# Performance work log

Measured on AMD Instinct MI355X. Metric: run time of the kernel, lower is better.

The kernel has to match this reference:

```python
import jax, jax.numpy as jnp
import numpy as np
from jax import lax

SCORE_THRESH = 0.05
NMS_THRESH = 0.5
DET_PER_IMG = 100
K_PRE = 2048  # pre-NMS candidate cap (batched_nms is never run on N*C dense candidates)
BBOX_XFORM_CLIP = float(np.log(1000.0 / 16.0))
WX, WY, WW, WH = 10.0, 10.0, 5.0, 5.0


def _decode(reg, props):
    # reg: [N, C, 4] deltas, props: [N, 4] xyxy -> [N, C, 4] xyxy (torchvision BoxCoder.decode)
    w = props[:, 2] - props[:, 0]
    h = props[:, 3] - props[:, 1]
    cx = props[:, 0] + 0.5 * w
    cy = props[:, 1] + 0.5 * h
    dx = reg[..., 0] / WX
    dy = reg[..., 1] / WY
    dw = jnp.minimum(reg[..., 2] / WW, BBOX_XFORM_CLIP)
    dh = jnp.minimum(reg[..., 3] / WH, BBOX_XFORM_CLIP)
    pcx = dx * w[:, None] + cx[:, None]
    pcy = dy * h[:, None] + cy[:, None]
    pw = jnp.exp(dw) * w[:, None]
    ph = jnp.exp(dh) * h[:, None]
    return jnp.stack([pcx - 0.5 * pw, pcy - 0.5 * ph, pcx + 0.5 * pw, pcy + 0.5 * ph], axis=-1)


def _pairwise_iou(b):
    # b: [K, 4] -> [K, K]
    area = (b[:, 2] - b[:, 0]) * (b[:, 3] - b[:, 1])
    lt = jnp.maximum(b[:, None, :2], b[None, :, :2])
    rb = jnp.minimum(b[:, None, 2:], b[None, :, 2:])
    wh = jnp.clip(rb - lt, 0.0)
    inter = wh[..., 0] * wh[..., 1]
    return inter / (area[:, None] + area[None, :] - inter)


def _greedy_nms(iou, valid, thresh):
    # boxes assumed sorted by descending score; valid: [K] bool initial keep mask
    K = iou.shape[0]
    idx = jnp.arange(K)
    def body(i, keep):
        sup = (iou[i] > thresh) & (idx > i) & keep[i]
        return keep & (~sup)
    return lax.fori_loop(0, K, body, valid)


def _process_image(logits, reg, props, img_h, img_w):
    # logits: [N, C], reg: [N, 4C], props: [N, 4]
    N, C = logits.shape
    scores = jax.nn.softmax(logits, axis=-1)[:, 1:]          # [N, C-1] drop background
    boxes = _decode(reg.reshape(N, C, 4), props)[:, 1:]      # [N, C-1, 4]
    boxes = jnp.stack([
        jnp.clip(boxes[..., 0], 0.0, img_w),
        jnp.clip(boxes[..., 1], 0.0, img_h),
        jnp.clip(boxes[..., 2], 0.0, img_w),
        jnp.clip(boxes[..., 3], 0.0, img_h),
    ], axis=-1)
    labels = jnp.broadcast_to(jnp.arange(1, C), (N, C - 1))
    boxes = boxes.reshape(-1, 4)       # [M, 4], M = N*(C-1)
    scores = scores.reshape(-1)
    labels = labels.reshape(-1)
    wd = boxes[:, 2] - boxes[:, 0]
    ht = boxes[:, 3] - boxes[:, 1]
    valid = (scores > SCORE_THRESH) & (wd >= 1.0) & (ht >= 1.0)  # score thresh + remove_small_boxes
    masked = jnp.where(valid, scores, -1.0)
    top_s, top_i = lax.top_k(masked, K_PRE)
    tb = boxes[top_i]
    tl = labels[top_i]
    tvalid = top_s > SCORE_THRESH
    # batched_nms via per-class coordinate offsets
    off = tl.astype(tb.dtype) * (jnp.max(tb) + 1.0)
    keep = _greedy_nms(_pairwise_iou(tb + off[:, None]), tvalid, NMS_THRESH)
    ks = jnp.where(keep, top_s, -1.0)
    fs, fi = lax.top_k(ks, DET_PER_IMG)
    fvalid = fs > SCORE_THRESH
    out_boxes = jnp.where(fvalid[:, None], tb[fi], 0.0)
    out_scores = jnp.where(fvalid, fs, 0.0)
    out_labels = jnp.where(fvalid, tl[fi], -1)
    return out_boxes, out_scores, out_labels


def setup_inputs() -> dict:
    key = jax.random.key(0)
    k1, k2, k3 = jax.random.split(key, 3)
    B, N, C, H, W = 8, 4000, 91, 800, 800
    pts = jax.random.uniform(k1, (B, N, 2, 2), dtype=jnp.float32, minval=0.0, maxval=float(W))
    proposals = jnp.concatenate([pts.min(axis=2), pts.max(axis=2)], axis=-1)  # valid xyxy
    class_logits = jax.random.normal(k2, (B * N, C), dtype=jnp.float32)
    box_regression = 0.5 * jax.random.normal(k3, (B * N, 4 * C), dtype=jnp.float32)
    return {"class_logits": class_logits, "box_regression": box_regression,
            "proposals": proposals, "img_h": H, "img_w": W}


def reference(class_logits, box_regression, proposals, img_h, img_w):
    B, N, _ = proposals.shape
    C = class_logits.shape[-1]
    logits = class_logits.reshape(B, N, C)
    reg = box_regression.reshape(B, N, 4 * C)
    fn = lambda l, r, p: _process_image(l, r, p, float(img_h), float(img_w))
    boxes, scores, labels = jax.vmap(fn)(logits, reg, proposals)
    return boxes, scores, labels
```

## Files before the change

### kernel.cpp

```cpp
#include <hip/hip_runtime.h>
#include <stdint.h>

typedef unsigned int u32;
typedef unsigned long long u64;
typedef __attribute__((ext_vector_type(2))) unsigned long long u64x2;

#define BIMG 8
#define NPROP 4000
#define NCLS 91
#define CM1 90
#define MCAND (NPROP * CM1)
#define KPRE 2048
#define NBUCKET 4096
#define NREP 8
#define SELCAP 16384
#define NSLOT 32
#define DETS 100
#define WLCAP 2048
#define SCORE_T 0.05f
#define NMS_T 0.5f
#define BBOX_CLIP 4.135166556742356f

#define HISTREP_OFF ((size_t)0)
#define BCNTREP_OFF (HISTREP_OFF + (size_t)NREP * BIMG * NBUCKET * 4)
#define META_OFF    (BCNTREP_OFF + (size_t)NREP * BIMG * NBUCKET * 4)
#define ZERO_BYTES  (META_OFF + 4096)
#define START_OFF   (ZERO_BYTES)
#define HISTTOT_OFF (START_OFF + (size_t)BIMG * NBUCKET * 4)
#define STARTREP_OFF (HISTTOT_OFF + (size_t)BIMG * NBUCKET * 4)
#define SEL_OFF     (STARTREP_OFF + (size_t)NREP * BIMG * NBUCKET * 4)
#define TBOX_OFF    (SEL_OFF + (size_t)BIMG * SELCAP * 8)
#define TSB_OFF     (TBOX_OFF + (size_t)BIMG * KPRE * 16)
#define TSC_OFF     (TSB_OFF + (size_t)BIMG * KPRE * 16)
#define TLB_OFF     (TSC_OFF + (size_t)BIMG * KPRE * 4)
#define TVLB_OFF    (TLB_OFF + (size_t)BIMG * KPRE * 4)
#define WLIST_OFF   (TVLB_OFF + (size_t)BIMG * 32 * 8)
#define CLIST_OFF   (WLIST_OFF + (size_t)BIMG * WLCAP * 4)
#define CVALID_OFF  (CLIST_OFF + (size_t)BIMG * NPROP * NSLOT * 8)
#define MASK_OFF    (CVALID_OFF + (size_t)BIMG * NPROP * 2 * 8)
#define WS_NEED     (MASK_OFF + (size_t)BIMG * KPRE * 32 * 8)

__device__ __forceinline__ void decode_clip(const float4 rg, const float w, const float h,
                                            const float cx, const float cy,
                                            const float fw, const float fh, float bx[4]) {
    float dx = rg.x / 10.0f;
    float dy = rg.y / 10.0f;
    float dw = fminf(rg.z / 5.0f, BBOX_CLIP);
    float dh = fminf(rg.w / 5.0f, BBOX_CLIP);
    float pcx = dx * w + cx;
    float pcy = dy * h + cy;
    float pw  = expf(dw) * w;
    float phh = expf(dh) * h;
    bx[0] = fminf(fmaxf(pcx - 0.5f * pw,  0.0f), fw);
    bx[1] = fminf(fmaxf(pcy - 0.5f * phh, 0.0f), fh);
    bx[2] = fminf(fmaxf(pcx + 0.5f * pw,  0.0f), fw);
    bx[3] = fminf(fmaxf(pcy + 0.5f * phh, 0.0f), fh);
}

__global__ __launch_bounds__(256) void k1_score_hist(
    const float* __restrict__ logits, const float* __restrict__ reg,
    const float* __restrict__ props, const int* __restrict__ imh, const int* __restrict__ imw,
    u32* __restrict__ histrep, u64* __restrict__ clist, u64* __restrict__ cvalid) {
    const int lane = threadIdx.x & 63;
    const int pid = blockIdx.x * 4 + (threadIdx.x >> 6);
    if (pid >= BIMG * NPROP) return;
    const int img = pid / NPROP;
    const float fw = (float)imw[0], fh = (float)imh[0];
    const float* lrow = logits + (size_t)pid * NCLS;
    float v0 = lrow[lane];
    float v1 = (lane < 27) ? lrow[lane + 64] : -3.0e38f;
    float mx = fmaxf(v0, v1);
#pragma unroll
    for (int o = 32; o > 0; o >>= 1) mx = fmaxf(mx, __shfl_xor(mx, o));
    float es = expf(v0 - mx) + ((lane < 27) ? expf(v1 - mx) : 0.0f);
#pragma unroll
    for (int o = 32; o > 0; o >>= 1) es += __shfl_xor(es, o);
    const float thr = mx + logf(es) - 2.9967323f;
    float4 p = reinterpret_cast<const float4*>(props)[pid];
    const float w = p.z - p.x, h = p.w - p.y;
    const float cx = p.x + 0.5f * w, cy = p.y + 0.5f * h;
    const float4* rrow = reinterpret_cast<const float4*>(reg) + (size_t)pid * NCLS;
    const int n = pid - img * NPROP;
    const int rep = n & (NREP - 1);
    const float sh0 = __shfl(v0, (lane + 1) & 63);
    const float sh1 = __shfl(v1, (lane + 1) & 63);
    u64 w0 = 0ull, w1 = 0ull;
    u32 base1 = 0;
#pragma unroll
    for (int batch = 0; batch < 2; ++batch) {
        const int ci = lane + batch * 64;
        bool valid = false;
        u32 ob = 0u;
        if (ci < CM1) {
            const float l = (batch == 0) ? ((lane == 63) ? sh1 : sh0) : sh1;
            if (l > thr) {
                float sc = expf(l - mx) / es;
                float4 rg = rrow[ci + 1];
                float bx[4];
                decode_clip(rg, w, h, cx, cy, fw, fh, bx);
                valid = (sc > SCORE_T) && (bx[2] - bx[0] >= 1.0f) && (bx[3] - bx[1] >= 1.0f);
                if (valid) {
                    ob = __float_as_uint(sc) | 0x80000000u;
                    atomicAdd(&histrep[((size_t)img * NREP + rep) * NBUCKET + (ob >> 20)], 1u);
                }
            }
        }
        const u64 bal = __ballot(valid);
        if (batch == 0) { w0 = bal; base1 = (u32)__popcll(bal); }
        else            { w1 = bal; }
        if (valid) {
            const u32 pre = (u32)__popcll(bal & ((1ull << lane) - 1ull));
            const u32 slot = (batch == 0) ? pre : (base1 + pre);
            const u32 idx = (u32)n * CM1 + (u32)ci;
            clist[(size_t)pid * NSLOT + slot] = ((u64)ob << 32) | (u32)(~idx);
        }
    }
    if (lane == 0) {
        u64x2 v; v.x = w0; v.y = w1;
        reinterpret_cast<u64x2*>(cvalid)[pid] = v;
    }
}

__global__ __launch_bounds__(256) void k2_scan(
    const u32* __restrict__ histrep, u32* __restrict__ histtot,
    u32* __restrict__ start, u32* __restrict__ startrep, u32* __restrict__ meta,
    u32* __restrict__ wlist) {
    __shared__ u32 wsum[4], qws[4];
    __shared__ u32 TbkS, Vs;
    const int img = blockIdx.x;
    const int td = threadIdx.x;
    const int ln = td & 63, wv = td >> 6;
    const int lo = 4080 - td * 16;
    u32 cnt[16];
#pragma unroll
    for (int k = 0; k < 16; ++k) cnt[k] = 0;
    const u32* hb = histrep + (size_t)img * NREP * NBUCKET + lo;
#pragma unroll
    for (int r = 0; r < NREP; ++r) {
        const uint4* q = reinterpret_cast<const uint4*>(hb + (size_t)r * NBUCKET);
        uint4 a = q[0], b = q[1], c = q[2], d = q[3];
        cnt[15] += a.x; cnt[14] += a.y; cnt[13] += a.z; cnt[12] += a.w;
        cnt[11] += b.x; cnt[10] += b.y; cnt[9]  += b.z; cnt[8]  += b.w;
        cnt[7]  += c.x; cnt[6]  += c.y; cnt[5]  += c.z; cnt[4]  += c.w;
        cnt[3]  += d.x; cnt[2]  += d.y; cnt[1]  += d.z; cnt[0]  += d.w;
    }
    u32 tsum = 0;
#pragma unroll
    for (int k = 0; k < 16; ++k) tsum += cnt[k];
    u32 inc = tsum;
#pragma unroll
    for (int o = 1; o < 64; o <<= 1) { u32 t = __shfl_up(inc, o); if (ln >= o) inc += t; }
    if (td == 0) TbkS = 0u;
    if (ln == 63) wsum[wv] = inc;
    __syncthreads();
    u32 wbase = 0;
    for (int i = 0; i < wv; ++i) wbase += wsum[i];
    if (td == 255) Vs = wbase + inc;
    const u32 excl0 = wbase + inc - tsum;
    u32 sub[16];
    u32 excl = excl0;
#pragma unroll
    for (int k = 0; k < 16; ++k) {
        const int bk = 4095 - (td * 16 + k);
        start[img * NBUCKET + bk] = excl;
        histtot[img * NBUCKET + bk] = cnt[k];
        sub[k] = excl;
        if (cnt[k] > 0 && excl < KPRE && excl + cnt[k] >= KPRE) TbkS = (u32)bk;
        excl += cnt[k];
    }
#pragma unroll
    for (int r = 0; r < NREP; ++r) {
        const uint4* q = reinterpret_cast<const uint4*>(hb + (size_t)r * NBUCKET);
        uint4 a = q[0], b = q[1], c = q[2], d = q[3];
        u32 hh[16] = { d.w, d.z, d.y, d.x, c.w, c.z, c.y, c.x,
                       b.w, b.z, b.y, b.x, a.w, a.z, a.y, a.x };
#pragma unroll
        for (int k = 0; k < 16; ++k) {
            const int bk = 4095 - (td * 16 + k);
            startrep[((size_t)img * NBUCKET + bk) * NREP + r] = sub[k];
            sub[k] += hh[k];
        }
    }
    u32 qcnt = 0;
    {
        u32 e = excl0;
#pragma unroll
        for (int k = 0; k < 16; ++k) { if (cnt[k] >= 2 && e < KPRE) ++qcnt; e += cnt[k]; }
    }
    u32 qinc = qcnt;
#pragma unroll
    for (int o = 1; o < 64; o <<= 1) { u32 t = __shfl_up(qinc, o); if (ln >= o) qinc += t; }
    if (ln == 63) qws[wv] = qinc;
    __syncthreads();
    u32 qbase = 0;
    for (int i = 0; i < wv; ++i) qbase += qws[i];
    u32 qoff = qbase + qinc - qcnt;
    {
        u32 e = excl0;
#pragma unroll
        for (int k = 0; k < 16; ++k) {
            const int bk = 4095 - (td * 16 + k);
            if (cnt[k] >= 2 && e < KPRE && qoff < WLCAP) wlist[img * WLCAP + (qoff++)] = (u32)bk;
            e += cnt[k];
        }
    }
    if (td == 255) meta[img * 8 + 3] = qbase + qinc;
    __syncthreads();
    if (td == 0) {
        u32 V = Vs;
        meta[img * 8 + 0] = V;
        meta[img * 8 + 1] = TbkS;
        meta[img * 8 + 2] = (V < KPRE) ? (KPRE - V) : 0u;
    }
}

__global__ __launch_bounds__(256) void k3_compact(
    const u64* __restrict__ clist, const u64* __restrict__ cvalid,
    const u32* __restrict__ startrep, const u32* __restrict__ meta,
    u32* __restrict__ bcntrep, u64* __restrict__ sel) {
    const u32 t = blockIdx.x * 256 + threadIdx.x;
    const u32 row = t >> 2;
    const u32 s0 = t & 3;
    if (row < (u32)(BIMG * NPROP)) {
        const u64x2 vb = reinterpret_cast<const u64x2*>(cvalid)[row];
        const u32 rcnt = (u32)__popcll(vb.x) + (u32)__popcll(vb.y);
        if (s0 < rcnt) {
            const u32 img = row / NPROP;
            const u32 n = row - img * NPROP;
            const u32 rep = n & (NREP - 1);
            const u32 cutoff = meta[img * 8 + 1];
            for (u32 slot = s0; slot < rcnt; slot += 4) {
                const u64 e = clist[(size_t)row * NSLOT + slot];
                const u32 bk = (u32)(e >> 52);
                if (bk >= cutoff) {
                    const u32 pos = startrep[((size_t)img * NBUCKET + bk) * NREP + rep] +
                        atomicAdd(&bcntrep[((size_t)rep * BIMG + img) * NBUCKET + bk], 1u);
                    if (pos < SELCAP) sel[(size_t)img * SELCAP + pos] = e;
                }
            }
        }
    }
    if (blockIdx.x < BIMG && threadIdx.x < 64) {
        const int img = blockIdx.x;
        const u32 need = meta[img * 8 + 2];
        if (need != 0) {
            const u32 V = meta[img * 8 + 0];
            const int lv = threadIdx.x;
            const u32 ORDN1 = 0x407FFFFFu;
            u32 filled = 0;
            for (u32 b0 = 0; b0 < MCAND && filled < need; b0 += 64) {
                const u32 idx = b0 + (u32)lv;
                bool inv = false;
                if (idx < MCAND) {
                    const u32 nn = (u32)(((u64)idx * 3054198967ull) >> 38);
                    const u32 cq = idx - nn * 90u;
                    const u64 wb = cvalid[((size_t)img * NPROP + nn) * 2 + (cq >> 6)];
                    inv = ((wb >> (cq & 63)) & 1ull) == 0ull;
                }
                const u64 bal = __ballot(inv);
                const u32 pre = (u32)__popcll(bal & ((1ull << lv) - 1ull));
                if (inv && (filled + pre) < need)
                    sel[(size_t)img * SELCAP + V + filled + pre] =
                        ((u64)ORDN1 << 32) | (u32)(~idx);
                filled += (u32)__popcll(bal);
            }
        }
    }
}

__global__ __launch_bounds__(256) void k4_sortseg(
    const u32* __restrict__ histtot, const u32* __restrict__ start,
    const u32* __restrict__ meta, const u32* __restrict__ wlist, u64* __restrict__ sel) {
    __shared__ u64 arr[4096];
    const int img = blockIdx.y;
    const int tid = threadIdx.x;
    const u32 wcount = meta[img * 8 + 3];
    for (u32 wi = blockIdx.x; wi < wcount; wi += gridDim.x) {
        const u32 bk = (wi < WLCAP) ? wlist[img * WLCAP + wi] : 0u;
        u32 cnt = histtot[img * NBUCKET + bk];
        u32 st = start[img * NBUCKET + bk];
        if (cnt <= 64 || st >= KPRE) continue;
        if (st + cnt > SELCAP) cnt = SELCAP - st;
        if (cnt > 4096) cnt = 4096;
        int n = 1;
        while (n < (int)cnt) n <<= 1;
        u64* seg = sel + (size_t)img * SELCAP + st;
        for (int i = tid; i < n; i += 256) arr[i] = (i < (int)cnt) ? seg[i] : 0ull;
        __syncthreads();
        for (int k = 2; k <= n; k <<= 1)
            for (int j = k >> 1; j > 0; j >>= 1) {
                for (int i = tid; i < n; i += 256) {
                    int ixj = i ^ j;
                    if (ixj > i) {
                        u64 a = arr[i], b = arr[ixj];
                        bool swp = ((i & k) == 0) ? (a < b) : (a > b);
                        if (swp) { arr[i] = b; arr[ixj] = a; }
                    }
                }
                __syncthreads();
            }
        for (int i = tid; i < (int)cnt; i += 256) seg[i] = arr[i];
        __syncthreads();
    }
    const int wv = tid >> 6, lane = tid & 63;
    for (u32 wi = blockIdx.x * 4 + wv; wi < wcount; wi += gridDim.x * 4) {
        const u32 bk = (wi < WLCAP) ? wlist[img * WLCAP + wi] : 0u;
        u32 cnt = histtot[img * NBUCKET + bk];
        u32 st = start[img * NBUCKET + bk];
        if (cnt < 2 || cnt > 64 || st >= KPRE) continue;
        if (st + cnt > SELCAP) cnt = SELCAP - st;
        u64* seg = sel + (size_t)img * SELCAP + st;
        u64 key = (lane < (int)cnt) ? seg[lane] : 0ull;
#pragma unroll
        for (int k = 2; k <= 64; k <<= 1) {
#pragma unroll
            for (int j = k >> 1; j > 0; j >>= 1) {
                u64 other = __shfl_xor(key, j);
                bool takeMax = ((lane & j) == 0) == ((lane & k) == 0);
                u64 hi2 = (key > other) ? key : other;
                u64 lo2 = (key > other) ? other : key;
                key = takeMax ? hi2 : lo2;
            }
        }
        if (lane < (int)cnt) seg[lane] = key;
    }
}

__global__ __launch_bounds__(1024) void k5_gather(
    const u64* __restrict__ sel, const float* __restrict__ reg, const float* __restrict__ props,
    const int* __restrict__ imh, const int* __restrict__ imw,
    float* __restrict__ tbox, float* __restrict__ tsb, float* __restrict__ tsc,
    int* __restrict__ tlb, u64* __restrict__ tvlb) {
    const int img = blockIdx.x;
    const int tid = threadIdx.x;
    const float fw = (float)imw[0], fh = (float)imh[0];
    float bx[2][4];
    int lab[2];
    float lm = -3.0e38f;
#pragma unroll
    for (int t = 0; t < 2; ++t) {
        int s = t * 1024 + tid;
        u64 key = sel[(size_t)img * SELCAP + s];
        u32 o = (u32)(key >> 32);
        u32 idx = ~((u32)key);
        u32 b = (o & 0x80000000u) ? (o & 0x7FFFFFFFu) : ~o;
        float sc = __uint_as_float(b);
        u32 n = idx / CM1;
        int c = (int)(idx - n * CM1) + 1;
        int pid = img * NPROP + (int)n;
        float4 p = reinterpret_cast<const float4*>(props)[pid];
        float w = p.z - p.x, h = p.w - p.y;
        float cx = p.x + 0.5f * w, cy = p.y + 0.5f * h;
        float4 rg = reinterpret_cast<const float4*>(reg)[(size_t)pid * NCLS + c];
        decode_clip(rg, w, h, cx, cy, fw, fh, bx[t]);
        lab[t] = c;
        lm = fmaxf(lm, fmaxf(fmaxf(bx[t][0], bx[t][1]), fmaxf(bx[t][2], bx[t][3])));
        reinterpret_cast<float4*>(tbox)[(size_t)img * KPRE + s] =
            make_float4(bx[t][0], bx[t][1], bx[t][2], bx[t][3]);
        tsc[(size_t)img * KPRE + s] = sc;
        tlb[(size_t)img * KPRE + s] = c;
        u64 bw = __ballot(sc > SCORE_T);
        if ((tid & 63) == 0) tvlb[img * 32 + t * 16 + (tid >> 6)] = bw;
    }
#pragma unroll
    for (int o2 = 32; o2 > 0; o2 >>= 1) lm = fmaxf(lm, __shfl_xor(lm, o2));
    __shared__ float wm[16];
    if ((tid & 63) == 0) wm[tid >> 6] = lm;
    __syncthreads();
    float m = wm[0];
#pragma unroll
    for (int i = 1; i < 16; ++i) m = fmaxf(m, wm[i]);
    const float mplus = m + 1.0f;
#pragma unroll
    for (int t = 0; t < 2; ++t) {
        int s = t * 1024 + tid;
        float off = (float)lab[t] * mplus;
        reinterpret_cast<float4*>(tsb)[(size_t)img * KPRE + s] =
            make_float4(bx[t][0] + off, bx[t][1] + off, bx[t][2] + off, bx[t][3] + off);
    }
}

__global__ __launch_bounds__(256) void k6_mask(
    const float* __restrict__ tsb, u64* __restrict__ mask) {
    const int img = blockIdx.y;
    const int wv = threadIdx.x >> 6, lane = threadIdx.x & 63;
    const u32 t = blockIdx.x * 4 + wv;
    float f = sqrtf(8.0f * (float)t + 1.0f);
    u32 x = (u32)((f - 1.0f) * 0.5f);
    while ((x + 1) * (x + 2) / 2 <= t) ++x;
    while (x * (x + 1) / 2 > t) --x;
    const u32 y = t - x * (x + 1) / 2;
    const int j0 = (int)x * 64;
    const int i0 = (int)y * 64;
    __shared__ float4 cb[4][64];
    __shared__ float ca[4][64];
    float4 c = reinterpret_cast<const float4*>(tsb)[(size_t)img * KPRE + j0 + lane];
    cb[wv][lane] = c;
    ca[wv][lane] = (c.z - c.x) * (c.w - c.y);
    __syncthreads();
    const int i = i0 + lane;
    float4 r = reinterpret_cast<const float4*>(tsb)[(size_t)img * KPRE + i];
    float ra = (r.z - r.x) * (r.w - r.y);
    u64 bits = 0ull;
#pragma unroll 8
    for (int jj = 0; jj < 64; ++jj) {
        int j = j0 + jj;
        float4 cc = cb[wv][jj];
        float wvv = fmaxf(fminf(r.z, cc.z) - fmaxf(r.x, cc.x), 0.0f);
        float hvv = fmaxf(fminf(r.w, cc.w) - fmaxf(r.y, cc.y), 0.0f);
        float inter = wvv * hvv;
        float iou = inter / ((ra + ca[wv][jj]) - inter);
        if ((iou > NMS_T) && (j > i)) bits |= (1ull << jj);
    }
    mask[((size_t)img * KPRE + i) * 32 + (j0 >> 6)] = bits;
}

__device__ __forceinline__ u64 rdlane64(u64 v, int l) {
    u32 lo = (u32)__builtin_amdgcn_readlane((int)(u32)v, l);
    u32 hi = (u32)__builtin_amdgcn_readlane((int)(u32)(v >> 32), l);
    return ((u64)hi << 32) | lo;
}

__device__ __forceinline__ void g2l16(const void* g, void* l) {
    __builtin_amdgcn_global_load_lds(
        (const __attribute__((address_space(1))) void*)g,
        (__attribute__((address_space(3))) void*)l, 16, 0, 0);
}

__global__ __launch_bounds__(64) void k7_nms_sel(
    const u64* __restrict__ mask, const u64* __restrict__ tvlb,
    const float* __restrict__ tsc, const float* __restrict__ tbox,
    const int* __restrict__ tlb, float* __restrict__ out) {
    __shared__ u64 smem[4096];
    const int img = blockIdx.x;
    const int lane = threadIdx.x;
    const int lg = lane >> 4;
    const int wlo = 2 * (lane & 15);
    const u64* mrow = mask + (size_t)img * KPRE * 32;

    u64 accx, accy, rp;
    {
        u64 nv = 0ull;
        if (lane < 32) nv = ~tvlb[img * 32 + lane];
        rp   = __shfl(nv, 0);
        accx = __shfl(nv, (lane & 15) * 2);
        accy = __shfl(nv, (lane & 15) * 2 + 1);
    }

    {
        const char* gsrc = (const char*)mrow + (size_t)lane * 16;
#pragma unroll
        for (int t = 0; t < 16; ++t)
            g2l16(gsrc + (size_t)t * 1024, (char*)smem + (size_t)t * 1024);
    }
    u64 diag = mrow[(size_t)lane * 32];

    u32 tk = 0;
    int bcut = 31;

#pragma unroll 1
    for (int b = 0; b < 32; ++b) {
        const size_t base32 = (size_t)b * 2048;
        const u64* cbuf = smem + (size_t)(b & 1) * 2048;

        u64 diagn = 0ull;
        if (b + 1 < 32) {
            diagn = mrow[base32 + 2048 + (size_t)lane * 32 + (b + 1)];
            const char* gsrc = (const char*)(mrow + base32 + 2048) + (size_t)lane * 16;
            char* nb_l = (char*)(smem + (size_t)((b + 1) & 1) * 2048);
#pragma unroll
            for (int t = 0; t < 16; ++t)
                g2l16(gsrc + (size_t)t * 1024, nb_l + (size_t)t * 1024);
        }

        u64 A = rp;
#pragma unroll
        for (int u = 0; u < 64; ++u) {
            u64 row = rdlane64(diag, u);
            if (!((A >> u) & 1ull)) A |= row;
        }
        const u64 keptw = ~A;

        if (b + 1 < 32) asm volatile("s_waitcnt vmcnt(17)" ::: "memory");
        else            asm volatile("s_waitcnt vmcnt(0)" ::: "memory");

        const u64 gx = (wlo >= b) ? ~0ull : 0ull;
        const u64 gy = (wlo + 1 >= b) ? ~0ull : 0ull;

#define LDV(K) u64x2 v##K = *(const u64x2*)&cbuf[128 * (K) + 2 * lane];
#define PRV(K) { u32 nib = (u32)(keptw >> (4 * (K))) & 15u; \
                 u32 kb = (nib >> lg) & 1u; \
                 accx |= kb ? (v##K.x & gx) : 0ull; accy |= kb ? (v##K.y & gy) : 0ull; }
        LDV(0) LDV(1) LDV(2) LDV(3)
        LDV(4) LDV(5) LDV(6) LDV(7)     PRV(0) PRV(1) PRV(2) PRV(3)
        LDV(8) LDV(9) LDV(10) LDV(11)   PRV(4) PRV(5) PRV(6) PRV(7)
        LDV(12) LDV(13) LDV(14) LDV(15) PRV(8) PRV(9) PRV(10) PRV(11)
        PRV(12) PRV(13) PRV(14) PRV(15)
#undef LDV
#undef PRV

        tk += (u32)__popcll(keptw);
        if (tk >= (u32)DETS) { bcut = b; break; }

        const int nb2 = b + 1;
        if (nb2 < 32) {
            u64 asel = (nb2 & 1) ? accy : accx;
            const int sl = (nb2 >> 1) & 15;
            rp = rdlane64(asel, sl) | rdlane64(asel, sl + 16) |
                 rdlane64(asel, sl + 32) | rdlane64(asel, sl + 48);
        }
        diag = diagn;
    }

    asm volatile("s_waitcnt vmcnt(0)" ::: "memory");

    accx |= __shfl_xor(accx, 16); accx |= __shfl_xor(accx, 32);
    accy |= __shfl_xor(accy, 16); accy |= __shfl_xor(accy, 32);

    u64 mxv = __shfl(accx, (lane >> 1) & 15);
    u64 myv = __shfl(accy, (lane >> 1) & 15);
    u64 kw = (lane & 1) ? ~myv : ~mxv;
    if (lane >= 32 || lane > bcut) kw = 0ull;

    u32 cnt = (u32)__popcll(kw);
    u32 inc = cnt;
#pragma unroll
    for (int o = 1; o < 64; o <<= 1) { u32 t = __shfl_up(inc, o); if (lane >= o) inc += t; }
    const u32 excl = inc - cnt;
    const u32 total = (u32)__shfl(inc, 63);

    float* ob0 = out + (size_t)img * DETS * 4;
    float* os0 = out + (size_t)BIMG * DETS * 4 + (size_t)img * DETS;
    float* ol0 = out + (size_t)BIMG * DETS * 5 + (size_t)img * DETS;

#pragma unroll
    for (int t = 0; t < 2; ++t) {
        u32 r = (u32)lane + (u32)t * 64;
        if (r < DETS && r >= total) {
            reinterpret_cast<float4*>(ob0)[r] = make_float4(0.f, 0.f, 0.f, 0.f);
            os0[r] = 0.0f;
            ol0[r] = -1.0f;
        }
    }
    u64 w = kw;
    u32 r = excl;
    while (w != 0ull && r < DETS) {
        int p = __ffsll((unsigned long long)w) - 1;
        w &= (w - 1ull);
        u32 s = (u32)lane * 64u + (u32)p;
        reinterpret_cast<float4*>(ob0)[r] =
            reinterpret_cast<const float4*>(tbox)[(size_t)img * KPRE + s];
        os0[r] = tsc[(size_t)img * KPRE + s];
        ol0[r] = (float)tlb[(size_t)img * KPRE + s];
        ++r;
    }
}

extern "C" void kernel_launch(void* const* d_in, const int* in_sizes, int n_in,
                              void* d_out, int out_size, void* d_ws, size_t ws_size,
                              hipStream_t stream) {
    const float* logits = (const float*)d_in[0];
    const float* reg    = (const float*)d_in[1];
    const float* props  = (const float*)d_in[2];
    const int*   imh    = (const int*)d_in[3];
    const int*   imw    = (const int*)d_in[4];
    float* out = (float*)d_out;
    char* ws = (char*)d_ws;
    if (ws_size < WS_NEED) return;

    u32* histrep  = (u32*)(ws + HISTREP_OFF);
    u32* bcntrep  = (u32*)(ws + BCNTREP_OFF);
    u32* meta     = (u32*)(ws + META_OFF);
    u32* start    = (u32*)(ws + START_OFF);
    u32* histtot  = (u32*)(ws + HISTTOT_OFF);
    u32* startrep = (u32*)(ws + STARTREP_OFF);
    u64* sel  = (u64*)(ws + SEL_OFF);
    float* tbox = (float*)(ws + TBOX_OFF);
    float* tsb  = (float*)(ws + TSB_OFF);
    float* tsc  = (float*)(ws + TSC_OFF);
    int*   tlb  = (int*)(ws + TLB_OFF);
    u64*   tvlb = (u64*)(ws + TVLB_OFF);
    u32*   wlist = (u32*)(ws + WLIST_OFF);
    u64*   clist = (u64*)(ws + CLIST_OFF);
    u64*   cvalid = (u64*)(ws + CVALID_OFF);
    u64*   mask = (u64*)(ws + MASK_OFF);

    hipMemsetAsync(d_ws, 0, ZERO_BYTES, stream);

    k1_score_hist<<<BIMG * NPROP / 4, 256, 0, stream>>>(logits, reg, props, imh, imw,
                                                        histrep, clist, cvalid);
    k2_scan<<<BIMG, 256, 0, stream>>>(histrep, histtot, start, startrep, meta, wlist);
    k3_compact<<<(BIMG * NPROP * 4) / 256, 256, 0, stream>>>(clist, cvalid, startrep,
                                                             meta, bcntrep, sel);
    k4_sortseg<<<dim3(64, BIMG), 256, 0, stream>>>(histtot, start, meta, wlist, sel);
    k5_gather<<<BIMG, 1024, 0, stream>>>(sel, reg, props, imh, imw, tbox, tsb, tsc, tlb, tvlb);
    k6_mask<<<dim3(132, BIMG), 256, 0, stream>>>(tsb, mask);
    k7_nms_sel<<<BIMG, 64, 0, stream>>>(mask, tvlb, tsc, tbox, tlb, out);
}
```

Before: 227.6 us.

## Fuse IoU mask build into NMS kernel computing blocks lazily in LDS

```diff
diff --git a/kernel.cpp b/kernel.cpp
--- a/kernel.cpp
+++ b/kernel.cpp
@@ -22,8 +22,7 @@
 #define BBOX_CLIP 4.135166556742356f
 
 #define HISTREP_OFF ((size_t)0)
-#define BCNTREP_OFF (HISTREP_OFF + (size_t)NREP * BIMG * NBUCKET * 4)
-#define META_OFF    (BCNTREP_OFF + (size_t)NREP * BIMG * NBUCKET * 4)
+#define META_OFF    (HISTREP_OFF + (size_t)NREP * BIMG * NBUCKET * 4)
 #define ZERO_BYTES  (META_OFF + 4096)
 #define START_OFF   (ZERO_BYTES)
 #define HISTTOT_OFF (START_OFF + (size_t)BIMG * NBUCKET * 4)
@@ -37,8 +36,7 @@
 #define WLIST_OFF   (TVLB_OFF + (size_t)BIMG * 32 * 8)
 #define CLIST_OFF   (WLIST_OFF + (size_t)BIMG * WLCAP * 4)
 #define CVALID_OFF  (CLIST_OFF + (size_t)BIMG * NPROP * NSLOT * 8)
-#define MASK_OFF    (CVALID_OFF + (size_t)BIMG * NPROP * 2 * 8)
-#define WS_NEED     (MASK_OFF + (size_t)BIMG * KPRE * 32 * 8)
+#define WS_NEED     (CVALID_OFF + (size_t)BIMG * NPROP * 2 * 8)
 
 __device__ __forceinline__ void decode_clip(const float4 rg, const float w, const float h,
                                             const float cx, const float cy,
@@ -177,7 +175,7 @@
 #pragma unroll
         for (int k = 0; k < 16; ++k) {
             const int bk = 4095 - (td * 16 + k);
-            startrep[((size_t)img * NBUCKET + bk) * NREP + r] = sub[k];
+            startrep[((size_t)r * BIMG + img) * NBUCKET + bk] = sub[k];
             sub[k] += hh[k];
         }
     }
@@ -216,8 +214,7 @@
 
 __global__ __launch_bounds__(256) void k3_compact(
     const u64* __restrict__ clist, const u64* __restrict__ cvalid,
-    const u32* __restrict__ startrep, const u32* __restrict__ meta,
-    u32* __restrict__ bcntrep, u64* __restrict__ sel) {
+    u32* __restrict__ startrep, const u32* __restrict__ meta, u64* __restrict__ sel) {
     const u32 t = blockIdx.x * 256 + threadIdx.x;
     const u32 row = t >> 2;
     const u32 s0 = t & 3;
@@ -233,8 +230,8 @@
                 const u64 e = clist[(size_t)row * NSLOT + slot];
                 const u32 bk = (u32)(e >> 52);
                 if (bk >= cutoff) {
-                    const u32 pos = startrep[((size_t)img * NBUCKET + bk) * NREP + rep] +
-                        atomicAdd(&bcntrep[((size_t)rep * BIMG + img) * NBUCKET + bk], 1u);
+                    const u32 pos =
+                        atomicAdd(&startrep[((size_t)rep * BIMG + img) * NBUCKET + bk], 1u);
                     if (pos < SELCAP) sel[(size_t)img * SELCAP + pos] = e;
                 }
             }
@@ -380,139 +377,111 @@
     }
 }
 
-__global__ __launch_bounds__(256) void k6_mask(
-    const float* __restrict__ tsb, u64* __restrict__ mask) {
-    const int img = blockIdx.y;
-    const int wv = threadIdx.x >> 6, lane = threadIdx.x & 63;
-    const u32 t = blockIdx.x * 4 + wv;
-    float f = sqrtf(8.0f * (float)t + 1.0f);
-    u32 x = (u32)((f - 1.0f) * 0.5f);
-    while ((x + 1) * (x + 2) / 2 <= t) ++x;
-    while (x * (x + 1) / 2 > t) --x;
-    const u32 y = t - x * (x + 1) / 2;
-    const int j0 = (int)x * 64;
-    const int i0 = (int)y * 64;
-    __shared__ float4 cb[4][64];
-    __shared__ float ca[4][64];
-    float4 c = reinterpret_cast<const float4*>(tsb)[(size_t)img * KPRE + j0 + lane];
-    cb[wv][lane] = c;
-    ca[wv][lane] = (c.z - c.x) * (c.w - c.y);
-    __syncthreads();
-    const int i = i0 + lane;
-    float4 r = reinterpret_cast<const float4*>(tsb)[(size_t)img * KPRE + i];
-    float ra = (r.z - r.x) * (r.w - r.y);
-    u64 bits = 0ull;
-#pragma unroll 8
-    for (int jj = 0; jj < 64; ++jj) {
-        int j = j0 + jj;
-        float4 cc = cb[wv][jj];
-        float wvv = fmaxf(fminf(r.z, cc.z) - fmaxf(r.x, cc.x), 0.0f);
-        float hvv = fmaxf(fminf(r.w, cc.w) - fmaxf(r.y, cc.y), 0.0f);
-        float inter = wvv * hvv;
-        float iou = inter / ((ra + ca[wv][jj]) - inter);
-        if ((iou > NMS_T) && (j > i)) bits |= (1ull << jj);
-    }
-    mask[((size_t)img * KPRE + i) * 32 + (j0 >> 6)] = bits;
-}
-
 __device__ __forceinline__ u64 rdlane64(u64 v, int l) {
     u32 lo = (u32)__builtin_amdgcn_readlane((int)(u32)v, l);
     u32 hi = (u32)__builtin_amdgcn_readlane((int)(u32)(v >> 32), l);
     return ((u64)hi << 32) | lo;
 }
 
-__device__ __forceinline__ void g2l16(const void* g, void* l) {
-    __builtin_amdgcn_global_load_lds(
-        (const __attribute__((address_space(1))) void*)g,
-        (__attribute__((address_space(3))) void*)l, 16, 0, 0);
-}
-
-__global__ __launch_bounds__(64) void k7_nms_sel(
-    const u64* __restrict__ mask, const u64* __restrict__ tvlb,
+__global__ __launch_bounds__(1024) void k67_nms(
+    const float* __restrict__ tsb, const u64* __restrict__ tvlb,
     const float* __restrict__ tsc, const float* __restrict__ tbox,
     const int* __restrict__ tlb, float* __restrict__ out) {
-    __shared__ u64 smem[4096];
+    __shared__ float4 bxl[2048];
+    __shared__ float  arl[2048];
+    __shared__ __align__(16) u64 msk[2048];
+    __shared__ u32 flag;
     const int img = blockIdx.x;
-    const int lane = threadIdx.x;
-    const int lg = lane >> 4;
-    const int wlo = 2 * (lane & 15);
-    const u64* mrow = mask + (size_t)img * KPRE * 32;
-
-    u64 accx, accy, rp;
-    {
-        u64 nv = 0ull;
-        if (lane < 32) nv = ~tvlb[img * 32 + lane];
-        rp   = __shfl(nv, 0);
-        accx = __shfl(nv, (lane & 15) * 2);
-        accy = __shfl(nv, (lane & 15) * 2 + 1);
-    }
-
-    {
-        const char* gsrc = (const char*)mrow + (size_t)lane * 16;
-#pragma unroll
-        for (int t = 0; t < 16; ++t)
-            g2l16(gsrc + (size_t)t * 1024, (char*)smem + (size_t)t * 1024);
-    }
-    u64 diag = mrow[(size_t)lane * 32];
-
+    const int tid = threadIdx.x;
+    const int wv = tid >> 6, ln = tid & 63;
+
+    for (int i = tid; i < KPRE; i += 1024) {
+        float4 c = reinterpret_cast<const float4*>(tsb)[(size_t)img * KPRE + i];
+        bxl[i] = c;
+        arl[i] = (c.z - c.x) * (c.w - c.y);
+    }
+    if (tid == 0) flag = 0;
+
+    u64 accx = 0ull, accy = 0ull, rp = 0ull;
     u32 tk = 0;
     int bcut = 31;
+    const int lg = ln >> 4;
+    const int wlo = 2 * (ln & 15);
+    if (wv == 0) {
+        u64 nv = 0ull;
+        if (ln < 32) nv = ~tvlb[img * 32 + ln];
+        rp   = __shfl(nv, 0);
+        accx = __shfl(nv, (ln & 15) * 2);
+        accy = __shfl(nv, (ln & 15) * 2 + 1);
+    }
+    __syncthreads();
 
 #pragma unroll 1
     for (int b = 0; b < 32; ++b) {
-        const size_t base32 = (size_t)b * 2048;
-        const u64* cbuf = smem + (size_t)(b & 1) * 2048;
-
-        u64 diagn = 0ull;
-        if (b + 1 < 32) {
-            diagn = mrow[base32 + 2048 + (size_t)lane * 32 + (b + 1)];
-            const char* gsrc = (const char*)(mrow + base32 + 2048) + (size_t)lane * 16;
-            char* nb_l = (char*)(smem + (size_t)((b + 1) & 1) * 2048);
-#pragma unroll
-            for (int t = 0; t < 16; ++t)
-                g2l16(gsrc + (size_t)t * 1024, nb_l + (size_t)t * 1024);
-        }
-
-        u64 A = rp;
-#pragma unroll
-        for (int u = 0; u < 64; ++u) {
-            u64 row = rdlane64(diag, u);
-            if (!((A >> u) & 1ull)) A |= row;
-        }
-        const u64 keptw = ~A;
-
-        if (b + 1 < 32) asm volatile("s_waitcnt vmcnt(17)" ::: "memory");
-        else            asm volatile("s_waitcnt vmcnt(0)" ::: "memory");
-
-        const u64 gx = (wlo >= b) ? ~0ull : 0ull;
-        const u64 gy = (wlo + 1 >= b) ? ~0ull : 0ull;
-
-#define LDV(K) u64x2 v##K = *(const u64x2*)&cbuf[128 * (K) + 2 * lane];
+        {
+            const int i = b * 64 + ln;
+            const float4 r = bxl[i];
+            const float ra = arl[i];
+            for (int x = b + wv; x < 32; x += 16) {
+                const int j0 = x * 64;
+                u64 bits = 0ull;
+#pragma unroll 8
+                for (int jj = 0; jj < 64; ++jj) {
+                    const int j = j0 + jj;
+                    float4 cc = bxl[j0 + jj];
+                    float wvv = fmaxf(fminf(r.z, cc.z) - fmaxf(r.x, cc.x), 0.0f);
+                    float hvv = fmaxf(fminf(r.w, cc.w) - fmaxf(r.y, cc.y), 0.0f);
+                    float inter = wvv * hvv;
+                    float iou = inter / ((ra + arl[j0 + jj]) - inter);
+                    if ((iou > NMS_T) && (j > i)) bits |= (1ull << jj);
+                }
+                msk[ln * 32 + x] = bits;
+            }
+        }
+        __syncthreads();
+        if (wv == 0) {
+            const u64 diag = msk[ln * 32 + b];
+            u64 A = rp;
+#pragma unroll
+            for (int u = 0; u < 64; ++u) {
+                u64 row = rdlane64(diag, u);
+                if (!((A >> u) & 1ull)) A |= row;
+            }
+            const u64 keptw = ~A;
+            const u64 gx = (wlo >= b) ? ~0ull : 0ull;
+            const u64 gy = (wlo + 1 >= b) ? ~0ull : 0ull;
+            const u64* cbuf = msk;
+#define LDV(K) u64x2 v##K = *(const u64x2*)&cbuf[128 * (K) + 2 * ln];
 #define PRV(K) { u32 nib = (u32)(keptw >> (4 * (K))) & 15u; \
                  u32 kb = (nib >> lg) & 1u; \
                  accx |= kb ? (v##K.x & gx) : 0ull; accy |= kb ? (v##K.y & gy) : 0ull; }
-        LDV(0) LDV(1) LDV(2) LDV(3)
-        LDV(4) LDV(5) LDV(6) LDV(7)     PRV(0) PRV(1) PRV(2) PRV(3)
-        LDV(8) LDV(9) LDV(10) LDV(11)   PRV(4) PRV(5) PRV(6) PRV(7)
-        LDV(12) LDV(13) LDV(14) LDV(15) PRV(8) PRV(9) PRV(10) PRV(11)
-        PRV(12) PRV(13) PRV(14) PRV(15)
+            LDV(0) LDV(1) LDV(2) LDV(3)
+            LDV(4) LDV(5) LDV(6) LDV(7)     PRV(0) PRV(1) PRV(2) PRV(3)
+            LDV(8) LDV(9) LDV(10) LDV(11)   PRV(4) PRV(5) PRV(6) PRV(7)
+            LDV(12) LDV(13) LDV(14) LDV(15) PRV(8) PRV(9) PRV(10) PRV(11)
+            PRV(12) PRV(13) PRV(14) PRV(15)
 #undef LDV
 #undef PRV
-
-        tk += (u32)__popcll(keptw);
-        if (tk >= (u32)DETS) { bcut = b; break; }
-
-        const int nb2 = b + 1;
-        if (nb2 < 32) {
-            u64 asel = (nb2 & 1) ? accy : accx;
-            const int sl = (nb2 >> 1) & 15;
-            rp = rdlane64(asel, sl) | rdlane64(asel, sl + 16) |
-                 rdlane64(asel, sl + 32) | rdlane64(asel, sl + 48);
-        }
-        diag = diagn;
-    }
-
-    asm volatile("s_waitcnt vmcnt(0)" ::: "memory");
+            tk += (u32)__popcll(keptw);
+            if (tk >= (u32)DETS) {
+                bcut = b;
+                if (ln == 0) flag = 1;
+            } else {
+                const int nb2 = b + 1;
+                if (nb2 < 32) {
+                    u64 asel = (nb2 & 1) ? accy : accx;
+                    const int sl = (nb2 >> 1) & 15;
+                    rp = rdlane64(asel, sl) | rdlane64(asel, sl + 16) |
+                         rdlane64(asel, sl + 32) | rdlane64(asel, sl + 48);
+                }
+            }
+        }
+        __syncthreads();
+        if (flag) break;
+    }
+
+    if (wv != 0) return;
+    const int lane = ln;
 
     accx |= __shfl_xor(accx, 16); accx |= __shfl_xor(accx, 32);
     accy |= __shfl_xor(accy, 16); accy |= __shfl_xor(accy, 32);
@@ -569,7 +538,6 @@
     if (ws_size < WS_NEED) return;
 
     u32* histrep  = (u32*)(ws + HISTREP_OFF);
-    u32* bcntrep  = (u32*)(ws + BCNTREP_OFF);
     u32* meta     = (u32*)(ws + META_OFF);
     u32* start    = (u32*)(ws + START_OFF);
     u32* histtot  = (u32*)(ws + HISTTOT_OFF);
@@ -583,7 +551,6 @@
     u32*   wlist = (u32*)(ws + WLIST_OFF);
     u64*   clist = (u64*)(ws + CLIST_OFF);
     u64*   cvalid = (u64*)(ws + CVALID_OFF);
-    u64*   mask = (u64*)(ws + MASK_OFF);
 
     hipMemsetAsync(d_ws, 0, ZERO_BYTES, stream);
 
@@ -591,9 +558,8 @@
                                                         histrep, clist, cvalid);
     k2_scan<<<BIMG, 256, 0, stream>>>(histrep, histtot, start, startrep, meta, wlist);
     k3_compact<<<(BIMG * NPROP * 4) / 256, 256, 0, stream>>>(clist, cvalid, startrep,
-                                                             meta, bcntrep, sel);
+                                                             meta, sel);
     k4_sortseg<<<dim3(64, BIMG), 256, 0, stream>>>(histtot, start, meta, wlist, sel);
     k5_gather<<<BIMG, 1024, 0, stream>>>(sel, reg, props, imh, imw, tbox, tsb, tsc, tlb, tvlb);
-    k6_mask<<<dim3(132, BIMG), 256, 0, stream>>>(tsb, mask);
-    k7_nms_sel<<<BIMG, 64, 0, stream>>>(mask, tvlb, tsc, tbox, tlb, out);
-}
+    k67_nms<<<BIMG, 1024, 0, stream>>>(tsb, tvlb, tsc, tbox, tlb, out);
+}
```

New measurement: 257.0 us. +12.9%, slower.
